# Kernel tuning notes

Hardware: AMD Instinct MI355X
Metric: run time of the kernel (lower is better)

Reference implementation:

```python
import jax, jax.numpy as jnp
import numpy as np

BS, M, CLIP_DIM = 64, 1000, 512
D = 512
N_WAYS = 20
N_Z = 8


def setup_inputs() -> dict:
    key = jax.random.key(0)
    ks = jax.random.split(key, 16)
    s = 0.02
    inp = {
        "x_context": jax.random.normal(ks[0], (BS, M, CLIP_DIM), jnp.float32),
        "y_context": jax.random.randint(ks[1], (BS, M), 0, N_WAYS),
        "x_query": jax.random.normal(ks[2], (BS, M, CLIP_DIM), jnp.float32),
        # image_proj
        "Wp": jax.random.normal(ks[3], (CLIP_DIM, D), jnp.float32) * s,
        "bp": jnp.zeros((D,), jnp.float32),
        # aggregator: Linear(d,d) -> GELU -> Linear(d,2d)
        "Wa1": jax.random.normal(ks[4], (D, D), jnp.float32) * s,
        "ba1": jnp.zeros((D,), jnp.float32),
        "Wa2": jax.random.normal(ks[5], (D, 2 * D), jnp.float32) * s,
        "ba2": jnp.zeros((2 * D,), jnp.float32),
        # decoder: Linear(d,d) -> GELU -> Linear(d,d)
        "Wd1": jax.random.normal(ks[6], (D, D), jnp.float32) * s,
        "bd1": jnp.zeros((D,), jnp.float32),
        "Wd2": jax.random.normal(ks[7], (D, D), jnp.float32) * s,
        "bd2": jnp.zeros((D,), jnp.float32),
    }
    return inp


def reference(x_context, y_context, x_query, Wp, bp, Wa1, ba1, Wa2, ba2, Wd1, bd1, Wd2, bd2):
    # project image embeddings: [bs, M, clip_dim] -> [bs, M, d]
    xc = x_context @ Wp + bp
    xq = x_query @ Wp + bp

    # encode_context_per_class: per-class masked sum == one-hot segment-sum
    # (original loops over classes doing (x*mask).sum(dim=1))
    oh = jax.nn.one_hot(y_context, N_WAYS, dtype=xc.dtype)  # [bs, M, N]
    r_C = jnp.einsum('bmn,bmd->bnd', oh, xc)  # [bs, N, d]

    # knowledge is None -> k = zeros; combined = relu(r + 0)
    combined = jax.nn.relu(r_C)
    h = jax.nn.gelu(combined @ Wa1 + ba1, approximate=False)
    stats = h @ Wa2 + ba2  # [bs, N, 2d]
    mu, scale_raw = stats[..., :D], stats[..., D:]
    scale = 0.01 + 0.99 * jax.nn.softplus(scale_raw)

    # eval path: sample n_z from q(z|C) via reparameterization
    eps = jax.random.normal(jax.random.key(42), (N_Z,) + mu.shape, mu.dtype)
    z_samples = mu[None] + scale[None] * eps  # [n_z, bs, N, d]

    # decode: class weight vectors then inner product with queries
    W = jax.nn.gelu(z_samples @ Wd1 + bd1, approximate=False) @ Wd2 + bd2
    logits = jnp.einsum('bqd,sbnd->sbqn', xq, W)  # [n_z, bs, Q*N, N]
    return logits, z_samples, mu, scale
```

## Files before the change

### kernel.cpp

```cpp
#include <hip/hip_runtime.h>
#include <hip/hip_bf16.h>
#include <stdint.h>


typedef __attribute__((ext_vector_type(8))) short short8;
typedef __attribute__((ext_vector_type(4))) float f32x4;

__device__ __forceinline__ float gelu_f(float x) {
    return 0.5f * x * (1.0f + erff(x * 0.70710678118654752440f));
}
__device__ __forceinline__ float softplus_f(float x) {
    return fmaxf(x, 0.0f) + log1pf(expf(-fabsf(x)));
}
__device__ __forceinline__ uint32_t cvt2(float a, float b) {
    __hip_bfloat162 h;
    h.x = __float2bfloat16(a);
    h.y = __float2bfloat16(b);
    uint32_t u; __builtin_memcpy(&u, &h, 4); return u;
}
__device__ __forceinline__ unsigned short f2bfu(float f) {
    __hip_bfloat16 h = __float2bfloat16(f);
    unsigned short u; __builtin_memcpy(&u, &h, 2); return u;
}
__device__ __forceinline__ float bfu2f(unsigned short u) {
    uint32_t v = (uint32_t)u << 16; float f; __builtin_memcpy(&f, &v, 4); return f;
}

__device__ __forceinline__ void threefry2x32(uint32_t k0, uint32_t k1,
                                             uint32_t x0, uint32_t x1,
                                             uint32_t& o0, uint32_t& o1) {
    uint32_t ks[3] = {k0, k1, k0 ^ k1 ^ 0x1BD11BDAu};
    x0 += ks[0]; x1 += ks[1];
    const uint32_t rot[8] = {13,15,26,6,17,29,16,24};
#pragma unroll
    for (int i = 0; i < 5; i++) {
#pragma unroll
        for (int j = 0; j < 4; j++) {
            uint32_t r = rot[(i & 1) * 4 + j];
            x0 += x1;
            x1 = (x1 << r) | (x1 >> (32 - r));
            x1 ^= x0;
        }
        x0 += ks[(i + 1) % 3];
        x1 += ks[(i + 2) % 3] + (uint32_t)(i + 1);
    }
    o0 = x0; o1 = x1;
}

__device__ __forceinline__ float bits_to_normal(uint32_t b) {
    float f = __uint_as_float((b >> 9) | 0x3F800000u) - 1.0f;
    const float lo = __uint_as_float(0xBF7FFFFFu);
    float u = fmaxf(lo, f * 2.0f + lo);
    return 1.41421356237309504880f * erfinvf(u);
}

__global__ __launch_bounds__(256) void prep_k(
    const float* __restrict__ Wp, const float* __restrict__ Wa1,
    const float* __restrict__ Wa2, const float* __restrict__ Wd1,
    const float* __restrict__ Wd2, const float* __restrict__ bp,
    const float* __restrict__ bd2, const int* __restrict__ y,
    unsigned short* __restrict__ WpTb, unsigned short* __restrict__ Wa1Tb,
    unsigned short* __restrict__ Wa2Tb, unsigned short* __restrict__ WdT1b,
    unsigned short* __restrict__ Wpb, unsigned short* __restrict__ Wd2b,
    float* __restrict__ bv, float* __restrict__ w2bp,
    float* __restrict__ c0, float* __restrict__ cnt)
{
    __shared__ float T[64][65];
    __shared__ int lc[32];
    __shared__ float ws4[4];
    const int f = blockIdx.x;
    const int tid = threadIdx.x;

    if (f < 320) {
        const float* src; unsigned short* dst; int C, t, xb, yb;
        if (f < 64)       { src = Wp;  dst = WpTb;  C = 512;  t = f;       xb = t & 7;  yb = t >> 3; }
        else if (f < 128) { src = Wa1; dst = Wa1Tb; C = 512;  t = f - 64;  xb = t & 7;  yb = t >> 3; }
        else if (f < 256) { src = Wa2; dst = Wa2Tb; C = 1024; t = f - 128; xb = t & 15; yb = t >> 4; }
        else              { src = Wd1; dst = WdT1b; C = 512;  t = f - 256; xb = t & 7;  yb = t >> 3; }
        const int r0 = yb * 64, cc0 = xb * 64;
        const int rr = tid >> 4, cc = (tid & 15) * 4;
#pragma unroll
        for (int l = 0; l < 4; l++) {
            int row = rr + l * 16;
            float4 v = *(const float4*)&src[(size_t)(r0 + row) * C + cc0 + cc];
            T[row][cc] = v.x; T[row][cc+1] = v.y; T[row][cc+2] = v.z; T[row][cc+3] = v.w;
        }
        __syncthreads();
#pragma unroll
        for (int l = 0; l < 4; l++) {
            int n = rr + l * 16;
            uint2 u;
            u.x = cvt2(T[cc][n], T[cc+1][n]);
            u.y = cvt2(T[cc+2][n], T[cc+3][n]);
            *(uint2*)&dst[(size_t)(cc0 + n) * 512 + r0 + cc] = u;
        }
    } else if (f < 576) {
        const float* src = (f < 448) ? Wp : Wd2;
        unsigned short* dst = (f < 448) ? Wpb : Wd2b;
        int t = (f < 448) ? f - 320 : f - 448;
        size_t i = ((size_t)t * 256 + tid) * 8;
        float4 a = *(const float4*)&src[i];
        float4 b4 = *(const float4*)&src[i + 4];
        uint4 u;
        u.x = cvt2(a.x, a.y);  u.y = cvt2(a.z, a.w);
        u.z = cvt2(b4.x, b4.y); u.w = cvt2(b4.z, b4.w);
        *(uint4*)&dst[i] = u;
    } else if (f < 832) {
        const float* W = (f < 704) ? Wp : Wd2;
        const float* v = (f < 704) ? bd2 : bp;
        float* o = (f < 704) ? bv : w2bp;
        int t = (f < 704) ? f - 576 : f - 704;
        int wave = tid >> 6, lane = tid & 63;
        int r = t * 4 + wave;
        const float* row = W + (size_t)r * 512 + lane * 8;
        float4 x0 = *(const float4*)row;
        float4 x1 = *(const float4*)(row + 4);
        float4 v0 = *(const float4*)&v[lane * 8];
        float4 v1 = *(const float4*)&v[lane * 8 + 4];
        float s = x0.x*v0.x + x0.y*v0.y + x0.z*v0.z + x0.w*v0.w
                + x1.x*v1.x + x1.y*v1.y + x1.z*v1.z + x1.w*v1.w;
#pragma unroll
        for (int off = 32; off > 0; off >>= 1) s += __shfl_down(s, off, 64);
        if (lane == 0) o[r] = s;
    } else if (f == 832) {
        float s = bp[tid] * bd2[tid] + bp[tid + 256] * bd2[tid + 256];
#pragma unroll
        for (int off = 32; off > 0; off >>= 1) s += __shfl_down(s, off, 64);
        int wave = tid >> 6, lane = tid & 63;
        if (lane == 0) ws4[wave] = s;
        __syncthreads();
        if (tid == 0) c0[0] = ws4[0] + ws4[1] + ws4[2] + ws4[3];
    } else {
        int b = f - 833;
        if (tid < 32) lc[tid] = 0;
        __syncthreads();
        for (int m = tid; m < 1000; m += 256)
            atomicAdd(&lc[y[b * 1000 + m]], 1);
        __syncthreads();
        if (tid < 20) cnt[b * 20 + tid] = (float)lc[tid];
    }
}

__global__ __launch_bounds__(512) void scatter_k(const float* __restrict__ xc,
                                                 const int* __restrict__ y,
                                                 float* __restrict__ Apart) {
    __shared__ float sA[20 * 512];
    const int b = blockIdx.x, ch = blockIdx.y;
    const int tid = threadIdx.x;
    for (int i = tid; i < 20 * 512; i += 512) sA[i] = 0.f;
    __syncthreads();
    const int m0 = ch * 125;
    const size_t xbase = ((size_t)b * 1000 + m0) * 512 + tid;
    const int ybase = b * 1000 + m0;

    float xv[8]; int cv[8];
#pragma unroll
    for (int j = 0; j < 8; j++) {
        xv[j] = xc[xbase + (size_t)j * 512];
        cv[j] = y[ybase + j];
    }
    int p = 8;
    for (int pan = 0; pan < 15; pan++) {
        float xn[8]; int cn[8];
        const bool more = (pan < 14);
        if (more) {
#pragma unroll
            for (int j = 0; j < 8; j++) {
                xn[j] = xc[xbase + (size_t)(p + j) * 512];
                cn[j] = y[ybase + p + j];
            }
        }
#pragma unroll
        for (int j = 0; j < 8; j++) sA[cv[j] * 512 + tid] += xv[j];
        if (more) {
#pragma unroll
            for (int j = 0; j < 8; j++) { xv[j] = xn[j]; cv[j] = cn[j]; }
            p += 8;
        }
    }
#pragma unroll
    for (int j = 0; j < 5; j++) {
        float xx = xc[xbase + (size_t)(120 + j) * 512];
        int cc = y[ybase + 120 + j];
        sA[cc * 512 + tid] += xx;
    }
    __syncthreads();
    float* dst = Apart + (size_t)ch * 655360 + (size_t)b * 10240;
    for (int i = tid; i < 10240; i += 512) dst[i] = sA[i];
}

__global__ __launch_bounds__(256) void reduce_bf_k(const float* __restrict__ Apart,
                                                   unsigned short* __restrict__ Abf) {
    int i = blockIdx.x * 256 + threadIdx.x;
    if (i < 163840) {
        const float4* Ap4 = (const float4*)Apart;
        float4 s = Ap4[i];
#pragma unroll
        for (int p = 1; p < 8; p++) {
            float4 v = Ap4[(size_t)p * 163840 + i];
            s.x += v.x; s.y += v.y; s.z += v.z; s.w += v.w;
        }
        uint2 o;
        o.x = cvt2(s.x, s.y); o.y = cvt2(s.z, s.w);
        *(uint2*)&Abf[(size_t)i * 4] = o;
    }
}

template <int EPI>
__global__ __launch_bounds__(256) void gm2_k(const unsigned short* __restrict__ Abf,
                                             const unsigned short* __restrict__ Bbf,
                                             const float* __restrict__ bias,
                                             const float* __restrict__ extra,
                                             unsigned short* __restrict__ C0,
                                             float* __restrict__ F0,
                                             float* __restrict__ F1,
                                             int Nn) {
    __shared__ unsigned short As[64 * 64];
    __shared__ unsigned short Bs[128 * 64];
    const int tid = threadIdx.x;
    const int lane = tid & 63, w = tid >> 6;
    const int row0 = blockIdx.y * 64, col0 = blockIdx.x * 128;
    f32x4 acc[4][2] = {};
    for (int k0 = 0; k0 < 512; k0 += 64) {
        {
            int row = tid >> 2, cs = (tid & 3) * 16;
            int swz = (row & 7) << 4;
            const unsigned short* src = Abf + (size_t)(row0 + row) * 512 + k0 + cs;
#pragma unroll
            for (int j = 0; j < 2; j++) {
                uint4 u = *(const uint4*)(src + j * 8);
                *(uint4*)((char*)As + row * 128 + (((cs + j * 8) * 2) ^ swz)) = u;
            }
        }
        {
            int row = tid >> 1, cs = (tid & 1) * 32;
            int swz = (row & 7) << 4;
            const unsigned short* src = Bbf + (size_t)(col0 + row) * 512 + k0 + cs;
#pragma unroll
            for (int j = 0; j < 4; j++) {
                uint4 u = *(const uint4*)(src + j * 8);
                *(uint4*)((char*)Bs + row * 128 + (((cs + j * 8) * 2) ^ swz)) = u;
            }
        }
        __syncthreads();
#pragma unroll
        for (int ks = 0; ks < 2; ks++) {
            short8 a[4], bb[2];
#pragma unroll
            for (int mi = 0; mi < 4; mi++) {
                int r = mi * 16 + (lane & 15);
                a[mi] = *(const short8*)((const char*)As + r * 128 +
                          (((ks * 32 + (lane >> 4) * 8) * 2) ^ ((r & 7) << 4)));
            }
#pragma unroll
            for (int ni = 0; ni < 2; ni++) {
                int n = w * 32 + ni * 16 + (lane & 15);
                bb[ni] = *(const short8*)((const char*)Bs + n * 128 +
                          (((ks * 32 + (lane >> 4) * 8) * 2) ^ ((n & 7) << 4)));
            }
#pragma unroll
            for (int mi = 0; mi < 4; mi++)
#pragma unroll
                for (int ni = 0; ni < 2; ni++)
                    acc[mi][ni] = __builtin_amdgcn_mfma_f32_16x16x32_bf16(a[mi], bb[ni], acc[mi][ni], 0, 0, 0);
        }
        __syncthreads();
    }
#pragma unroll
    for (int mi = 0; mi < 4; mi++) {
#pragma unroll
        for (int ni = 0; ni < 2; ni++) {
            int c = col0 + w * 32 + ni * 16 + (lane & 15);
            float bv = bias ? bias[c] : 0.f;
#pragma unroll
            for (int j = 0; j < 4; j++) {
                int r = row0 + mi * 16 + (lane >> 4) * 4 + j;
                float v = acc[mi][ni][j];
                if (EPI == 0) {
                    v += bv;
                    C0[(size_t)r * Nn + c] = f2bfu(v);
                } else if (EPI == 1) {
                    v += extra[r] * bv;
                    C0[(size_t)r * Nn + c] = f2bfu(fmaxf(v, 0.f));
                } else if (EPI == 2) {
                    C0[(size_t)r * Nn + c] = f2bfu(gelu_f(v + bv));
                } else {
                    v += bv;
                    if (c < 512) F0[(size_t)r * 512 + c] = v;
                    else F1[(size_t)r * 512 + (c - 512)] = 0.01f + 0.99f * softplus_f(v);
                }
            }
        }
    }
}

__global__ __launch_bounds__(256) void z2_k(const float* __restrict__ mu,
                                            const float* __restrict__ sc,
                                            float* __restrict__ z,
                                            unsigned short* __restrict__ zb) {
    const uint32_t NH = 2621440u;
    uint32_t i = blockIdx.x * 256u + threadIdx.x;
    if (i >= NH) return;
    uint32_t t0 = 2u * i;
    uint32_t o0, o1, p0, p1;
    threefry2x32(0u, 42u, 0u, t0, o0, o1);
    threefry2x32(0u, 42u, 0u, t0 + 1u, p0, p1);
    uint32_t r0 = t0 % 655360u;
    float2 mv = *(const float2*)&mu[r0];
    float2 sv = *(const float2*)&sc[r0];
    float z0 = mv.x + sv.x * bits_to_normal(o0 ^ o1);
    float z1 = mv.y + sv.y * bits_to_normal(p0 ^ p1);
    float2 zo; zo.x = z0; zo.y = z1;
    *(float2*)&z[t0] = zo;
    *(uint32_t*)&zb[t0] = cvt2(z0, z1);
}

__global__ __launch_bounds__(256) void beta2_k(const unsigned short* __restrict__ Wgb,
                                               const float* __restrict__ vec,
                                               const float* __restrict__ c0,
                                               float* __restrict__ beta) {
    int wave = threadIdx.x >> 6, lane = threadIdx.x & 63;
    int r = blockIdx.x * 4 + wave;
    short8 wv = *(const short8*)(Wgb + (size_t)r * 512 + lane * 8);
    float s = 0.f;
#pragma unroll
    for (int e = 0; e < 8; e++) s += vec[lane * 8 + e] * bfu2f((unsigned short)wv[e]);
#pragma unroll
    for (int o = 32; o > 0; o >>= 1) s += __shfl_down(s, o, 64);
    if (lane == 0) beta[r] = s + c0[0];
}

__global__ __launch_bounds__(512) void logits_mfma3_k(const float* __restrict__ Xq,
                                                      const unsigned short* __restrict__ Vb,
                                                      const float* __restrict__ beta,
                                                      float* __restrict__ out) {
    __shared__ unsigned short Vs[160 * 64];
    __shared__ float bs[160];
    const int u = blockIdx.x + 8 * blockIdx.y;
    const int xcd = u & 7, idx = u >> 3;
    const int b = (idx & 7) * 8 + xcd;
    const int qh = idx >> 3;
    const int tid = threadIdx.x, lane = tid & 63, w = tid >> 6;
    const int wq = w >> 1, wn = w & 1;

    if (tid < 160) {
        int s = tid / 20, n = tid - s * 20;
        bs[tid] = beta[(size_t)(s * 64 + b) * 20 + n];
    }

    const int klane = (lane >> 4) * 8;
    const float* xp[2];
    int qb[2];
#pragma unroll
    for (int qs = 0; qs < 2; qs++) {
        qb[qs] = qh * 128 + wq * 32 + qs * 16;
        int qr = qb[qs] + (lane & 15);
        if (qr > 999) qr = 999;
        xp[qs] = Xq + ((size_t)b * 1000 + qr) * 512 + klane;
    }
    int vrow[5], vswz[5];
#pragma unroll
    for (int nf = 0; nf < 5; nf++) {
        int rr = wn * 80 + nf * 16 + (lane & 15);
        vrow[nf] = rr * 128;
        vswz[nf] = (rr & 7) << 4;
    }

    f32x4 acc[2][5] = {};
    for (int k0 = 0; k0 < 512; k0 += 64) {
        __syncthreads();
        for (int c = tid; c < 640; c += 512) {
            int row = c >> 2, off = (c & 3) * 32;
            int sdiv = row / 20;
            int row_g = row + sdiv * 1260 + b * 20;
            const unsigned short* src = Vb + (size_t)row_g * 512 + k0 + (c & 3) * 16;
            uint4 u0 = *(const uint4*)src;
            uint4 u1 = *(const uint4*)(src + 8);
            int swz = (row & 7) << 4;
            char* base = (char*)Vs + row * 128;
            *(uint4*)(base + (off ^ swz)) = u0;
            *(uint4*)(base + ((off + 16) ^ swz)) = u1;
        }
        __syncthreads();
#pragma unroll
        for (int ks = 0; ks < 2; ks++) {
            int kb = (ks * 32 + klane) * 2;
            short8 bf[5];
#pragma unroll
            for (int nf = 0; nf < 5; nf++)
                bf[nf] = *(const short8*)((const char*)Vs + vrow[nf] + (kb ^ vswz[nf]));
            short8 af[2];
#pragma unroll
            for (int qs = 0; qs < 2; qs++) {
                const float* p = xp[qs] + k0 + ks * 32;
                float4 v0 = *(const float4*)p;
                float4 v1 = *(const float4*)(p + 4);
                uint4 uu;
                uu.x = cvt2(v0.x, v0.y); uu.y = cvt2(v0.z, v0.w);
                uu.z = cvt2(v1.x, v1.y); uu.w = cvt2(v1.z, v1.w);
                __builtin_memcpy(&af[qs], &uu, 16);
            }
#pragma unroll
            for (int qs = 0; qs < 2; qs++)
#pragma unroll
                for (int nf = 0; nf < 5; nf++)
                    acc[qs][nf] = __builtin_amdgcn_mfma_f32_16x16x32_bf16(af[qs], bf[nf], acc[qs][nf], 0, 0, 0);
        }
    }

#pragma unroll
    for (int nf = 0; nf < 5; nf++) {
        int rl = wn * 80 + nf * 16 + (lane & 15);
        int s = rl / 20, n = rl - s * 20;
        float bb = bs[rl];
        size_t ob = (size_t)(s * 64 + b) * 20000;
#pragma unroll
        for (int qs = 0; qs < 2; qs++) {
#pragma unroll
            for (int j = 0; j < 4; j++) {
                int q = qb[qs] + (lane >> 4) * 4 + j;
                if (q < 1000)
                    out[ob + (size_t)q * 20 + n] = acc[qs][nf][j] + bb;
            }
        }
    }
}

extern "C" void kernel_launch(void* const* d_in, const int* in_sizes, int n_in,
                              void* d_out, int out_size, void* d_ws, size_t ws_size,
                              hipStream_t stream) {
    const float* x_context = (const float*)d_in[0];
    const int*   y_context = (const int*)d_in[1];
    const float* x_query   = (const float*)d_in[2];
    const float* Wp  = (const float*)d_in[3];
    const float* bp  = (const float*)d_in[4];
    const float* Wa1 = (const float*)d_in[5];
    const float* ba1 = (const float*)d_in[6];
    const float* Wa2 = (const float*)d_in[7];
    const float* ba2 = (const float*)d_in[8];
    const float* Wd1 = (const float*)d_in[9];
    const float* bd1 = (const float*)d_in[10];
    const float* Wd2 = (const float*)d_in[11];
    const float* bd2 = (const float*)d_in[12];

    float* out    = (float*)d_out;
    float* logits = out;
    float* z      = out + 10240000;
    float* mu     = out + 15482880;
    float* sc     = out + 16138240;

    float* ws   = (float*)d_ws;
    float* cnt  = ws;
    float* beta = cnt + 1280;
    float* bv   = beta + 10240;
    float* w2bp = bv + 512;
    float* c0   = w2bp + 512;
    unsigned short* WpTb  = (unsigned short*)(c0 + 63);
    unsigned short* Wa1Tb = WpTb + 262144;
    unsigned short* Wa2Tb = Wa1Tb + 262144;
    unsigned short* WdT1b = Wa2Tb + 524288;
    unsigned short* Wpb   = WdT1b + 262144;
    unsigned short* Wd2b  = Wpb + 262144;
    unsigned short* Gtb   = Wd2b + 262144;
    unsigned short* Abf   = Gtb + 262144;
    unsigned short* combb = Abf + 655360;
    unsigned short* hb    = combb + 655360;
    unsigned short* zb    = hb + 655360;
    unsigned short* Vbf   = zb + 5242880;
    float* big = (float*)(Vbf + 5242880);
    unsigned short* Wgb = (unsigned short*)big;

    prep_k<<<dim3(897), 256, 0, stream>>>(Wp, Wa1, Wa2, Wd1, Wd2, bp, bd2, y_context,
                                          WpTb, Wa1Tb, Wa2Tb, WdT1b, Wpb, Wd2b,
                                          bv, w2bp, c0, cnt);
    gm2_k<0><<<dim3(4, 8), 256, 0, stream>>>(Wpb, Wd2b, nullptr, nullptr, Gtb, nullptr, nullptr, 512);
    scatter_k<<<dim3(64, 8), 512, 0, stream>>>(x_context, y_context, big );
    reduce_bf_k<<<dim3(640), 256, 0, stream>>>(big, Abf);
    gm2_k<1><<<dim3(4, 20), 256, 0, stream>>>(Abf, WpTb, bp, cnt, combb, nullptr, nullptr, 512);
    gm2_k<2><<<dim3(4, 20), 256, 0, stream>>>(combb, Wa1Tb, ba1, nullptr, hb, nullptr, nullptr, 512);
    gm2_k<3><<<dim3(8, 20), 256, 0, stream>>>(hb, Wa2Tb, ba2, nullptr, nullptr, mu, sc, 1024);
    z2_k<<<dim3(10240), 256, 0, stream>>>(mu, sc, z, zb);
    gm2_k<2><<<dim3(4, 160), 256, 0, stream>>>(zb, WdT1b, bd1, nullptr, Wgb, nullptr, nullptr, 512);
    gm2_k<0><<<dim3(4, 160), 256, 0, stream>>>(Wgb, Gtb, bv, nullptr, Vbf, nullptr, nullptr, 512);
    beta2_k<<<dim3(2560), 256, 0, stream>>>(Wgb, w2bp, c0, beta);
    logits_mfma3_k<<<dim3(8, 64), 512, 0, stream>>>(x_query, Vbf, beta, logits);
}
```

Measured before the change: 229.4 us.

## Compute per-class context sums as one-hot bf16 MFMA instead of scatter plus reduce

Replaces the LDS scatter-add kernel and the separate partial-sum reduction with a single kernel. It builds one-hot class fragments in registers and multiplies them against bf16-converted x_context tiles with MFMA, writing the bf16 class sums directly. This removes the fp32 partial-sum buffer round trip and one launch. The trade-off is that x values are rounded to bf16 before accumulation, the grid is smaller, and the loads are not software-pipelined, so the kernel may be more latency-bound. The bias variable rename in the GEMM epilogue is cosmetic.

Result: no change. 232.0 us (+1.1%).

```diff
diff --git a/kernel.cpp b/kernel.cpp
--- a/kernel.cpp
+++ b/kernel.cpp
@@ -141,68 +141,78 @@
     }
 }
 
-__global__ __launch_bounds__(512) void scatter_k(const float* __restrict__ xc,
-                                                 const int* __restrict__ y,
-                                                 float* __restrict__ Apart) {
-    __shared__ float sA[20 * 512];
-    const int b = blockIdx.x, ch = blockIdx.y;
-    const int tid = threadIdx.x;
-    for (int i = tid; i < 20 * 512; i += 512) sA[i] = 0.f;
-    __syncthreads();
-    const int m0 = ch * 125;
-    const size_t xbase = ((size_t)b * 1000 + m0) * 512 + tid;
-    const int ybase = b * 1000 + m0;
-
-    float xv[8]; int cv[8];
-#pragma unroll
-    for (int j = 0; j < 8; j++) {
-        xv[j] = xc[xbase + (size_t)j * 512];
-        cv[j] = y[ybase + j];
-    }
-    int p = 8;
-    for (int pan = 0; pan < 15; pan++) {
-        float xn[8]; int cn[8];
-        const bool more = (pan < 14);
-        if (more) {
-#pragma unroll
-            for (int j = 0; j < 8; j++) {
-                xn[j] = xc[xbase + (size_t)(p + j) * 512];
-                cn[j] = y[ybase + p + j];
-            }
-        }
-#pragma unroll
-        for (int j = 0; j < 8; j++) sA[cv[j] * 512 + tid] += xv[j];
-        if (more) {
-#pragma unroll
-            for (int j = 0; j < 8; j++) { xv[j] = xn[j]; cv[j] = cn[j]; }
-            p += 8;
-        }
-    }
-#pragma unroll
-    for (int j = 0; j < 5; j++) {
-        float xx = xc[xbase + (size_t)(120 + j) * 512];
-        int cc = y[ybase + 120 + j];
-        sA[cc * 512 + tid] += xx;
-    }
-    __syncthreads();
-    float* dst = Apart + (size_t)ch * 655360 + (size_t)b * 10240;
-    for (int i = tid; i < 10240; i += 512) dst[i] = sA[i];
-}
-
-__global__ __launch_bounds__(256) void reduce_bf_k(const float* __restrict__ Apart,
-                                                   unsigned short* __restrict__ Abf) {
-    int i = blockIdx.x * 256 + threadIdx.x;
-    if (i < 163840) {
-        const float4* Ap4 = (const float4*)Apart;
-        float4 s = Ap4[i];
-#pragma unroll
-        for (int p = 1; p < 8; p++) {
-            float4 v = Ap4[(size_t)p * 163840 + i];
-            s.x += v.x; s.y += v.y; s.z += v.z; s.w += v.w;
-        }
-        uint2 o;
-        o.x = cvt2(s.x, s.y); o.y = cvt2(s.z, s.w);
-        *(uint2*)&Abf[(size_t)i * 4] = o;
+__global__ __launch_bounds__(256) void onehot_k(const float* __restrict__ xc,
+                                                const int* __restrict__ y,
+                                                unsigned short* __restrict__ Abf) {
+    __shared__ unsigned short Xs[128 * 64];
+    __shared__ int ys[1024];
+    const int chb = blockIdx.x * 128;
+    const int b = blockIdx.y;
+    const int tid = threadIdx.x, lane = tid & 63, w = tid >> 6;
+    const int chs = w * 32;
+
+    for (int i = tid; i < 1024; i += 256)
+        ys[i] = (i < 1000) ? y[b * 1000 + i] : -1;
+
+    f32x4 acc[2][2] = {};
+    for (int step = 0; step < 16; step++) {
+        const int k0 = step * 64;
+        int m = k0 + lane; if (m > 999) m = 999;
+        const float* src = xc + ((size_t)b * 1000 + m) * 512 + chb + chs;
+        float x[32];
+#pragma unroll
+        for (int j8 = 0; j8 < 8; j8++) {
+            float4 v = *(const float4*)(src + j8 * 4);
+            x[j8*4+0]=v.x; x[j8*4+1]=v.y; x[j8*4+2]=v.z; x[j8*4+3]=v.w;
+        }
+        __syncthreads();
+#pragma unroll
+        for (int j = 0; j < 32; j++) {
+            int ch = chs + j;
+            *(unsigned short*)((char*)Xs + ch * 128 + ((lane * 2) ^ ((ch & 7) << 4)))
+                = f2bfu(x[j]);
+        }
+        __syncthreads();
+#pragma unroll
+        for (int ks = 0; ks < 2; ks++) {
+            int kb = ks * 32 + (lane >> 4) * 8;
+            int4 yv0 = *(const int4*)&ys[k0 + kb];
+            int4 yv1 = *(const int4*)&ys[k0 + kb + 4];
+            int ya[8] = {yv0.x, yv0.y, yv0.z, yv0.w, yv1.x, yv1.y, yv1.z, yv1.w};
+            short8 a[2];
+#pragma unroll
+            for (int mi = 0; mi < 2; mi++) {
+                int cls = mi * 16 + (lane & 15);
+#pragma unroll
+                for (int e = 0; e < 8; e++)
+                    a[mi][e] = (short)((ya[e] == cls) ? 0x3F80 : 0);
+            }
+            short8 bb[2];
+#pragma unroll
+            for (int ni = 0; ni < 2; ni++) {
+                int ch = chs + ni * 16 + (lane & 15);
+                bb[ni] = *(const short8*)((const char*)Xs + ch * 128 +
+                           ((kb * 2) ^ ((ch & 7) << 4)));
+            }
+#pragma unroll
+            for (int mi = 0; mi < 2; mi++)
+#pragma unroll
+                for (int ni = 0; ni < 2; ni++)
+                    acc[mi][ni] = __builtin_amdgcn_mfma_f32_16x16x32_bf16(a[mi], bb[ni], acc[mi][ni], 0, 0, 0);
+        }
+    }
+#pragma unroll
+    for (int mi = 0; mi < 2; mi++) {
+#pragma unroll
+        for (int ni = 0; ni < 2; ni++) {
+            int ch = chb + chs + ni * 16 + (lane & 15);
+#pragma unroll
+            for (int j = 0; j < 4; j++) {
+                int cls = mi * 16 + (lane >> 4) * 4 + j;
+                if (cls < 20)
+                    Abf[((size_t)b * 20 + cls) * 512 + ch] = f2bfu(acc[mi][ni][j]);
+            }
+        }
     }
 }
 
@@ -271,21 +281,21 @@
 #pragma unroll
         for (int ni = 0; ni < 2; ni++) {
             int c = col0 + w * 32 + ni * 16 + (lane & 15);
-            float bv = bias ? bias[c] : 0.f;
+            float bvv = bias ? bias[c] : 0.f;
 #pragma unroll
             for (int j = 0; j < 4; j++) {
                 int r = row0 + mi * 16 + (lane >> 4) * 4 + j;
                 float v = acc[mi][ni][j];
                 if (EPI == 0) {
-                    v += bv;
+                    v += bvv;
                     C0[(size_t)r * Nn + c] = f2bfu(v);
                 } else if (EPI == 1) {
-                    v += extra[r] * bv;
+                    v += extra[r] * bvv;
                     C0[(size_t)r * Nn + c] = f2bfu(fmaxf(v, 0.f));
                 } else if (EPI == 2) {
-                    C0[(size_t)r * Nn + c] = f2bfu(gelu_f(v + bv));
+                    C0[(size_t)r * Nn + c] = f2bfu(gelu_f(v + bvv));
                 } else {
-                    v += bv;
+                    v += bvv;
                     if (c < 512) F0[(size_t)r * 512 + c] = v;
                     else F1[(size_t)r * 512 + (c - 512)] = 0.01f + 0.99f * softplus_f(v);
                 }
@@ -474,8 +484,7 @@
                                           WpTb, Wa1Tb, Wa2Tb, WdT1b, Wpb, Wd2b,
                                           bv, w2bp, c0, cnt);
     gm2_k<0><<<dim3(4, 8), 256, 0, stream>>>(Wpb, Wd2b, nullptr, nullptr, Gtb, nullptr, nullptr, 512);
-    scatter_k<<<dim3(64, 8), 512, 0, stream>>>(x_context, y_context, big );
-    reduce_bf_k<<<dim3(640), 256, 0, stream>>>(big, Abf);
+    onehot_k<<<dim3(4, 64), 256, 0, stream>>>(x_context, y_context, Abf);
     gm2_k<1><<<dim3(4, 20), 256, 0, stream>>>(Abf, WpTb, bp, cnt, combb, nullptr, nullptr, 512);
     gm2_k<2><<<dim3(4, 20), 256, 0, stream>>>(combb, Wa1Tb, ba1, nullptr, hb, nullptr, nullptr, 512);
     gm2_k<3><<<dim3(8, 20), 256, 0, stream>>>(hb, Wa2Tb, ba2, nullptr, nullptr, mu, sc, 1024);
```
